# Performance work log

Hardware: AMD Instinct MI355X
Metric: run time of the kernel (lower is better)

The kernel has to match this reference:

```python
import jax, jax.numpy as jnp
from jax import lax
import numpy as np

L, B, D = 2048, 8, 1024
LN_EPS = 1e-5


def setup_inputs() -> dict:
    key = jax.random.key(0)
    k1, k2 = jax.random.split(key)
    x = jax.random.normal(k1, (L, B, D), dtype=jnp.float32)
    c0 = jnp.zeros((B, D), dtype=jnp.float32)
    # nn.Linear(D, 3D, bias=False): weight shape (3D, D), y = x @ W.T
    W = jax.random.normal(k2, (3 * D, D), dtype=jnp.float32) * (1.0 / np.sqrt(D))
    ln_w = jnp.ones((D,), dtype=jnp.float32)
    ln_b = jnp.zeros((D,), dtype=jnp.float32)
    return {"x": x, "c0": c0, "W": W, "ln_w": ln_w, "ln_b": ln_b}


def reference(x, c0, W, ln_w, ln_b):
    # ufr = x @ W.T : (L,B,3D)
    ufr = jnp.einsum('lbd,ed->lbe', x, W)
    u, f, r = jnp.split(ufr, 3, axis=-1)
    f = jax.nn.sigmoid(f)
    r = jax.nn.sigmoid(r)

    # sequential SRU recurrence: c_t = f_t * c_{t-1} + (1 - f_t) * u_t
    def step(c, fu):
        f_t, u_t = fu
        c = f_t * c + (1.0 - f_t) * u_t
        return c, c

    last_c, c_stack = lax.scan(step, c0, (f, u))  # c_stack: (L,B,D)

    hs = r * jnp.tanh(c_stack) + (1.0 - r) * x
    g = jax.nn.gelu(hs, approximate=False)  # torch F.gelu default = exact erf

    mu = jnp.mean(g, axis=-1, keepdims=True)
    var = jnp.mean(jnp.square(g - mu), axis=-1, keepdims=True)
    out = (g - mu) * lax.rsqrt(var + LN_EPS) * ln_w + ln_b
    return (out, last_c)
```

## Files before the change

kernel.cpp:

```cpp
#include <hip/hip_runtime.h>

typedef unsigned short u16;
typedef unsigned int   u32;
typedef __attribute__((ext_vector_type(8))) __bf16 bf16x8;
typedef __attribute__((ext_vector_type(4))) float  f32x4;

#define L_SEQ  2048
#define BATCH  8
#define DIM    1024
#define ROWS   16384
#define N3     3072
#define NCHUNK 64
#define LCHUNK 32
#define NCHAIN 8192

__device__ __forceinline__ float b2f(u16 h) {
  return __builtin_bit_cast(float, (u32)h << 16);
}
__device__ __forceinline__ u32 pk2(float a, float b) {
  u32 r;
  asm("v_cvt_pk_bf16_f32 %0, %1, %2" : "=v"(r) : "v"(a), "v"(b));
  return r;
}
__device__ __forceinline__ u16 f2b(float f) {
  u32 u = __builtin_bit_cast(u32, f);
  return (u16)((u + 0x7fffu + ((u >> 16) & 1u)) >> 16);
}
__device__ __forceinline__ f32x4 mf(bf16x8 a, bf16x8 b, f32x4 c) {
  return __builtin_amdgcn_mfma_f32_16x16x32_bf16(a, b, c, 0, 0, 0);
}

__global__ void k_pack(const float* __restrict__ x, const float* __restrict__ W,
                       u16* __restrict__ apk, u16* __restrict__ wpk) {
  const int NA = 128 * 32 * 8 * 64;
  const int NB = 12 * 32 * 16 * 64;
  int i = blockIdx.x * 256 + threadIdx.x;
  const int stride = gridDim.x * 256;
  for (; i < NA + NB; i += stride) {
    const float* src; u16* dst;
    if (i < NA) {
      int lane = i & 63, fg = (i >> 6) & 7, t = (i >> 9) & 31, mt = i >> 14;
      int row = mt * 128 + fg * 16 + (lane & 15);
      int k   = t * 32 + (lane >> 4) * 8;
      src = x + (size_t)row * DIM + k;
      dst = apk + (size_t)i * 8;
    } else {
      int j = i - NA;
      int lane = j & 63, c = (j >> 6) & 15, t = (j >> 10) & 31, nt = j >> 15;
      int col = nt * 256 + c * 16 + (lane & 15);
      int k   = t * 32 + (lane >> 4) * 8;
      src = W + (size_t)col * DIM + k;
      dst = wpk + (size_t)j * 8;
    }
    float4 v0 = *(const float4*)src;
    float4 v1 = *(const float4*)(src + 4);
    uint4 o;
    o.x = pk2(v0.x, v0.y); o.y = pk2(v0.z, v0.w);
    o.z = pk2(v1.x, v1.y); o.w = pk2(v1.z, v1.w);
    *(uint4*)dst = o;
  }
}

__device__ __forceinline__ void gl_lds16(const u16* g, u16* l) {
  __builtin_amdgcn_global_load_lds((const __attribute__((address_space(1))) void*)g,
                                   (__attribute__((address_space(3))) void*)l,
                                   16, 0, 0);
}

__global__ __launch_bounds__(512, 4) void k_gemm_v6(const u16* __restrict__ apk,
                                                    const u16* __restrict__ wpk,
                                                    u16* __restrict__ C) {
  __shared__ u16 lds[12288];
  const int tid  = threadIdx.x;
  const int lane = tid & 63;
  const int wid  = tid >> 6;
  const int wm = wid >> 2, wn = wid & 3;
  const int lr = lane & 15, lk = lane >> 4;

  const int bid = blockIdx.x;
  const int xcd = bid & 7;
  const int r   = bid >> 3;
  const int byl = r / 12;
  const int bx  = r - byl * 12;
  const int by  = xcd * 16 + byl;

  const u16* srcA = apk + ((((size_t)by * 32) * 8 + wid) * 64 + lane) * 8;
  const u16* srcB = wpk + ((((size_t)bx * 32) * 16 + wn * 4) * 64 + lane) * 8;

  u16* d0 = &lds[wid * 512 + lane * 8];
  u16* d1 = d0 + 4096;
  u16* d2 = d0 + 8192;
  const u16* ldsA = &lds[wm * 2048 + lane * 8];

  f32x4 acc[4][4] = {};
  bf16x8 A0, A1, A2, A3, B0, B1, B2, B3;

  {
    const u16* gb = srcB;
    A0 = *(const bf16x8*)(gb);
    A1 = *(const bf16x8*)(gb + 512);
    A2 = *(const bf16x8*)(gb + 1024);
    A3 = *(const bf16x8*)(gb + 1536);
  }
  __builtin_amdgcn_sched_barrier(0);
  gl_lds16(srcA, d0);
  gl_lds16(srcA + 4096, d1);
  asm volatile("s_waitcnt vmcnt(1)" ::: "memory");
  asm volatile("s_barrier" ::: "memory");

#define GBODY(T, RB, DN, U0,U1,U2,U3, L0,L1,L2,L3, LOADB, STAGEA, LASTP) {   \
    if (STAGEA) gl_lds16(srcA + (size_t)((T) + 2) * 4096, DN);               \
    __builtin_amdgcn_sched_barrier(0);                                       \
    if (LOADB) {                                                             \
      const u16* gb_ = srcB + (size_t)((T) + 1) * 8192;                      \
      L0 = *(const bf16x8*)(gb_);                                            \
      L1 = *(const bf16x8*)(gb_ + 512);                                      \
      L2 = *(const bf16x8*)(gb_ + 1024);                                     \
      L3 = *(const bf16x8*)(gb_ + 1536);                                     \
    }                                                                        \
    __builtin_amdgcn_sched_barrier(0);                                       \
    const u16* rb_ = ldsA + (RB) * 4096;                                     \
    bf16x8 av0 = *(const bf16x8*)(rb_);                                      \
    bf16x8 av1 = *(const bf16x8*)(rb_ + 512);                                \
    bf16x8 av2 = *(const bf16x8*)(rb_ + 1024);                               \
    bf16x8 av3 = *(const bf16x8*)(rb_ + 1536);                               \
    __builtin_amdgcn_s_setprio(1);                                           \
    acc[0][0]=mf(av0,U0,acc[0][0]); acc[0][1]=mf(av0,U1,acc[0][1]);          \
    acc[0][2]=mf(av0,U2,acc[0][2]); acc[0][3]=mf(av0,U3,acc[0][3]);          \
    acc[1][0]=mf(av1,U0,acc[1][0]); acc[1][1]=mf(av1,U1,acc[1][1]);          \
    acc[1][2]=mf(av1,U2,acc[1][2]); acc[1][3]=mf(av1,U3,acc[1][3]);          \
    acc[2][0]=mf(av2,U0,acc[2][0]); acc[2][1]=mf(av2,U1,acc[2][1]);          \
    acc[2][2]=mf(av2,U2,acc[2][2]); acc[2][3]=mf(av2,U3,acc[2][3]);          \
    acc[3][0]=mf(av3,U0,acc[3][0]); acc[3][1]=mf(av3,U1,acc[3][1]);          \
    acc[3][2]=mf(av3,U2,acc[3][2]); acc[3][3]=mf(av3,U3,acc[3][3]);          \
    __builtin_amdgcn_s_setprio(0);                                           \
    if (!(LASTP)) asm volatile("s_barrier" ::: "memory");                    \
  }

  for (int t6 = 0; t6 < 30; t6 += 6) {
    GBODY(t6 + 0, 0, d2, A0,A1,A2,A3, B0,B1,B2,B3, 1, 1, 0)
    GBODY(t6 + 1, 1, d0, B0,B1,B2,B3, A0,A1,A2,A3, 1, 1, 0)
    GBODY(t6 + 2, 2, d1, A0,A1,A2,A3, B0,B1,B2,B3, 1, 1, 0)
    GBODY(t6 + 3, 0, d2, B0,B1,B2,B3, A0,A1,A2,A3, 1, 1, 0)
    GBODY(t6 + 4, 1, d0, A0,A1,A2,A3, B0,B1,B2,B3, 1, 1, 0)
    GBODY(t6 + 5, 2, d1, B0,B1,B2,B3, A0,A1,A2,A3, 1, 1, 0)
  }
  GBODY(30, 0, d2, A0,A1,A2,A3, B0,B1,B2,B3, 1, 0, 0)
  GBODY(31, 1, d0, B0,B1,B2,B3, A0,A1,A2,A3, 0, 0, 1)
#undef GBODY

  const bool act = (bx >= 4);
#pragma unroll
  for (int m = 0; m < 4; ++m) {
    const int row0 = by * 128 + wm * 64 + m * 16 + lk * 4;
#pragma unroll
    for (int n = 0; n < 4; ++n) {
      const int col = bx * 256 + wn * 64 + n * 16 + lr;
#pragma unroll
      for (int j = 0; j < 4; ++j) {
        float v = acc[m][n][j];
        if (act) v = 1.f / (1.f + __expf(-v));
        C[(size_t)(row0 + j) * N3 + col] = f2b(v);
      }
    }
  }
}

__global__ __launch_bounds__(256) void k_gemm_reg(const float* __restrict__ A,
                                                  const float* __restrict__ B,
                                                  u16* __restrict__ C) {
  __shared__ u16 lds[8192];
  const int tid  = threadIdx.x;
  const int lane = tid & 63;
  const int wid  = tid >> 6;
  const int wm = wid >> 1, wn = wid & 1;
  const int lr = lane & 15, lk = lane >> 4;
  const int mBase = blockIdx.y << 7;
  const int nBase = blockIdx.x << 7;

  f32x4 acc[4][4] = {};
  const int aoff = (wm * 64 + lr) * 32 + lk * 8;
  const int boff = 4096 + (wn * 64 + lr) * 32 + lk * 8;

  for (int k0 = 0; k0 < DIM; k0 += 32) {
#pragma unroll
    for (int q = 0; q < 4; ++q) {
      const int i  = q * 256 + tid;
      const int rr = i >> 3;
      const int cc = (i & 7) << 2;
      float4 va = *(const float4*)(A + (size_t)(mBase + rr) * DIM + k0 + cc);
      float4 vb = *(const float4*)(B + (size_t)(nBase + rr) * DIM + k0 + cc);
      uint2 pa; pa.x = pk2(va.x, va.y); pa.y = pk2(va.z, va.w);
      uint2 pb; pb.x = pk2(vb.x, vb.y); pb.y = pk2(vb.z, vb.w);
      *(uint2*)&lds[rr * 32 + cc] = pa;
      *(uint2*)&lds[4096 + rr * 32 + cc] = pb;
    }
    __syncthreads();
    bf16x8 av[4], bv[4];
#pragma unroll
    for (int m = 0; m < 4; ++m) av[m] = *(const bf16x8*)&lds[aoff + m * 512];
#pragma unroll
    for (int n = 0; n < 4; ++n) bv[n] = *(const bf16x8*)&lds[boff + n * 512];
#pragma unroll
    for (int m = 0; m < 4; ++m)
#pragma unroll
      for (int n = 0; n < 4; ++n)
        acc[m][n] = mf(av[m], bv[n], acc[m][n]);
    __syncthreads();
  }

  const bool act = (nBase >= DIM);
#pragma unroll
  for (int m = 0; m < 4; ++m) {
    const int row0 = mBase + wm * 64 + m * 16 + lk * 4;
#pragma unroll
    for (int n = 0; n < 4; ++n) {
      const int col = nBase + wn * 64 + n * 16 + lr;
#pragma unroll
      for (int j = 0; j < 4; ++j) {
        float v = acc[m][n][j];
        if (act) v = 1.f / (1.f + __expf(-v));
        C[(size_t)(row0 + j) * N3 + col] = f2b(v);
      }
    }
  }
}

__global__ void k_scanA(const u16* __restrict__ ufr, float* __restrict__ P,
                        float* __restrict__ V) {
  int g = blockIdx.x * 256 + threadIdx.x;
  int j = g >> 13;
  int chain = g & (NCHAIN - 1);
  int b = chain >> 10;
  int d = chain & (DIM - 1);
  const u16* p = ufr + (size_t)((j * LCHUNK) * BATCH + b) * N3 + d;
  float prod = 1.f, v = 0.f;
  for (int t = 0; t < LCHUNK; ++t) {
    float u = b2f(p[0]);
    float f = b2f(p[DIM]);
    v = f * v + (1.f - f) * u;
    prod *= f;
    p += BATCH * N3;
  }
  P[g] = prod; V[g] = v;
}

__global__ void k_scanB(const float* __restrict__ c0, const float* __restrict__ P,
                        const float* __restrict__ V, float* __restrict__ S,
                        float* __restrict__ lastc) {
  int chain = blockIdx.x * 256 + threadIdx.x;
  float c = c0[chain];
  for (int j = 0; j < NCHUNK; ++j) {
    S[j * NCHAIN + chain] = c;
    c = P[j * NCHAIN + chain] * c + V[j * NCHAIN + chain];
  }
  lastc[chain] = c;
}

__global__ __launch_bounds__(1024) void k_scanln(const u16* __restrict__ ufr,
                                                 const float* __restrict__ S,
                                                 const float* __restrict__ x,
                                                 const float* __restrict__ lnw,
                                                 const float* __restrict__ lnb,
                                                 float* __restrict__ out) {
  const int j = blockIdx.x >> 3;
  const int b = blockIdx.x & 7;
  const int d = threadIdx.x;
  const int lane = d & 63, wid = d >> 6;

  float c = S[j * NCHAIN + b * DIM + d];
  const float wgt = lnw[d];
  const float bia = lnb[d];

  const u16*   pu = ufr + (size_t)((j * LCHUNK) * BATCH + b) * N3 + d;
  const float* px = x   + (size_t)((j * LCHUNK) * BATCH + b) * DIM + d;
  float*       po = out + (size_t)((j * LCHUNK) * BATCH + b) * DIM + d;

  __shared__ float red1[16], red2[16];

  u16 cu = pu[0], cf = pu[DIM], cr = pu[2 * DIM];
  float cx = *px;

  for (int t = 0; t < LCHUNK; ++t) {
    const int adv = (t < LCHUNK - 1) ? 1 : 0;
    u16 nu = pu[(size_t)adv * BATCH * N3];
    u16 nf = pu[(size_t)adv * BATCH * N3 + DIM];
    u16 nr = pu[(size_t)adv * BATCH * N3 + 2 * DIM];
    float nx = px[(size_t)adv * BATCH * DIM];

    float u = b2f(cu), f = b2f(cf), rr = b2f(cr), xx = cx;
    c = f * c + (1.f - f) * u;
    float hs = rr * tanhf(c) + (1.f - rr) * xx;
    float g  = 0.5f * hs * (1.f + erff(hs * 0.70710678118654752f));

    float s1 = g, s2 = g * g;
#pragma unroll
    for (int off = 32; off > 0; off >>= 1) {
      s1 += __shfl_down(s1, off, 64);
      s2 += __shfl_down(s2, off, 64);
    }
    if (lane == 0) { red1[wid] = s1; red2[wid] = s2; }
    __syncthreads();
    float S1 = 0.f, S2 = 0.f;
#pragma unroll
    for (int w = 0; w < 16; ++w) { S1 += red1[w]; S2 += red2[w]; }
    float mu  = S1 * (1.f / DIM);
    float var = S2 * (1.f / DIM) - mu * mu;
    float inv = rsqrtf(var + 1e-5f);
    *po = (g - mu) * inv * wgt + bia;
    __syncthreads();

    cu = nu; cf = nf; cr = nr; cx = nx;
    pu += BATCH * N3;
    px += BATCH * DIM;
    po += BATCH * DIM;
  }
}

extern "C" void kernel_launch(void* const* d_in, const int* in_sizes, int n_in,
                              void* d_out, int out_size, void* d_ws, size_t ws_size,
                              hipStream_t stream) {
  (void)in_sizes; (void)n_in; (void)out_size;
  const float* x   = (const float*)d_in[0];
  const float* c0  = (const float*)d_in[1];
  const float* W   = (const float*)d_in[2];
  const float* lnw = (const float*)d_in[3];
  const float* lnb = (const float*)d_in[4];
  float* out   = (float*)d_out;
  float* lastc = out + (size_t)ROWS * DIM;

  char* ws = (char*)d_ws;

  u16* ufr; float *P, *V, *S;
  const size_t FULL_NEED = 140509184;
  if (ws_size >= FULL_NEED) {
    u16* apk = (u16*)ws;
    u16* wpk = (u16*)(ws + 33554432);
    ufr = (u16*)(ws + 39845888);
    P   = (float*)ws;
    V   = (float*)(ws + 2097152);
    S   = (float*)(ws + 4194304);
    k_pack<<<2048, 256, 0, stream>>>(x, W, apk, wpk);
    k_gemm_v6<<<1536, 512, 0, stream>>>(apk, wpk, ufr);
  } else {
    ufr = (u16*)ws;
    P   = (float*)(ws + 100663296);
    V   = (float*)(ws + 102760448);
    S   = (float*)(ws + 104857600);
    dim3 g1(N3 / 128, ROWS / 128);
    k_gemm_reg<<<g1, 256, 0, stream>>>(x, W, ufr);
  }

  k_scanA<<<(NCHUNK * NCHAIN) / 256, 256, 0, stream>>>(ufr, P, V);
  k_scanB<<<NCHAIN / 256, 256, 0, stream>>>(c0, P, V, S, lastc);
  k_scanln<<<NCHUNK * BATCH, 1024, 0, stream>>>(ufr, S, x, lnw, lnb, out);
}
```

Measured before the change: 234.4 us.

## Vectorize scan kernels to four channels per thread and halve chunk length

```diff
diff --git a/kernel.cpp b/kernel.cpp
--- a/kernel.cpp
+++ b/kernel.cpp
@@ -10,9 +10,11 @@
 #define DIM    1024
 #define ROWS   16384
 #define N3     3072
-#define NCHUNK 64
-#define LCHUNK 32
+#define NCHUNK 128
+#define LCHUNK 16
 #define NCHAIN 8192
+
+struct __align__(8) us4 { u16 x, y, z, w; };
 
 __device__ __forceinline__ float b2f(u16 h) {
   return __builtin_bit_cast(float, (u32)h << 16);
@@ -228,21 +230,27 @@
 
 __global__ void k_scanA(const u16* __restrict__ ufr, float* __restrict__ P,
                         float* __restrict__ V) {
-  int g = blockIdx.x * 256 + threadIdx.x;
-  int j = g >> 13;
-  int chain = g & (NCHAIN - 1);
-  int b = chain >> 10;
-  int d = chain & (DIM - 1);
-  const u16* p = ufr + (size_t)((j * LCHUNK) * BATCH + b) * N3 + d;
-  float prod = 1.f, v = 0.f;
+  int idx = blockIdx.x * 256 + threadIdx.x;
+  int j  = idx >> 11;
+  int cg = idx & 2047;
+  int b  = cg >> 8;
+  int d0 = (cg & 255) << 2;
+  const u16* p = ufr + (size_t)((j * LCHUNK) * BATCH + b) * N3 + d0;
+  float prod0 = 1.f, prod1 = 1.f, prod2 = 1.f, prod3 = 1.f;
+  float v0 = 0.f, v1 = 0.f, v2 = 0.f, v3 = 0.f;
   for (int t = 0; t < LCHUNK; ++t) {
-    float u = b2f(p[0]);
-    float f = b2f(p[DIM]);
-    v = f * v + (1.f - f) * u;
-    prod *= f;
+    us4 uu = *(const us4*)(p);
+    us4 ff = *(const us4*)(p + DIM);
+    float f0 = b2f(ff.x), f1 = b2f(ff.y), f2 = b2f(ff.z), f3 = b2f(ff.w);
+    v0 = f0 * v0 + (1.f - f0) * b2f(uu.x); prod0 *= f0;
+    v1 = f1 * v1 + (1.f - f1) * b2f(uu.y); prod1 *= f1;
+    v2 = f2 * v2 + (1.f - f2) * b2f(uu.z); prod2 *= f2;
+    v3 = f3 * v3 + (1.f - f3) * b2f(uu.w); prod3 *= f3;
     p += BATCH * N3;
   }
-  P[g] = prod; V[g] = v;
+  const int base = j * NCHAIN + b * DIM + d0;
+  *(float4*)&P[base] = make_float4(prod0, prod1, prod2, prod3);
+  *(float4*)&V[base] = make_float4(v0, v1, v2, v3);
 }
 
 __global__ void k_scanB(const float* __restrict__ c0, const float* __restrict__ P,
@@ -257,58 +265,89 @@
   lastc[chain] = c;
 }
 
-__global__ __launch_bounds__(1024) void k_scanln(const u16* __restrict__ ufr,
-                                                 const float* __restrict__ S,
-                                                 const float* __restrict__ x,
-                                                 const float* __restrict__ lnw,
-                                                 const float* __restrict__ lnb,
-                                                 float* __restrict__ out) {
+__global__ __launch_bounds__(256) void k_scanln(const u16* __restrict__ ufr,
+                                                const float* __restrict__ S,
+                                                const float* __restrict__ x,
+                                                const float* __restrict__ lnw,
+                                                const float* __restrict__ lnb,
+                                                float* __restrict__ out) {
   const int j = blockIdx.x >> 3;
   const int b = blockIdx.x & 7;
-  const int d = threadIdx.x;
-  const int lane = d & 63, wid = d >> 6;
-
-  float c = S[j * NCHAIN + b * DIM + d];
-  const float wgt = lnw[d];
-  const float bia = lnb[d];
-
-  const u16*   pu = ufr + (size_t)((j * LCHUNK) * BATCH + b) * N3 + d;
-  const float* px = x   + (size_t)((j * LCHUNK) * BATCH + b) * DIM + d;
-  float*       po = out + (size_t)((j * LCHUNK) * BATCH + b) * DIM + d;
-
-  __shared__ float red1[16], red2[16];
-
-  u16 cu = pu[0], cf = pu[DIM], cr = pu[2 * DIM];
-  float cx = *px;
+  const int tid = threadIdx.x;
+  const int d0 = tid << 2;
+  const int lane = tid & 63, wid = tid >> 6;
+
+  float4 c4  = *(const float4*)&S[j * NCHAIN + b * DIM + d0];
+  float c0v = c4.x, c1v = c4.y, c2v = c4.z, c3v = c4.w;
+  const float4 wv = *(const float4*)(lnw + d0);
+  const float4 bv = *(const float4*)(lnb + d0);
+
+  const u16*   pu = ufr + (size_t)((j * LCHUNK) * BATCH + b) * N3 + d0;
+  const float* px = x   + (size_t)((j * LCHUNK) * BATCH + b) * DIM + d0;
+  float*       po = out + (size_t)((j * LCHUNK) * BATCH + b) * DIM + d0;
+
+  __shared__ float red1[2][4], red2[2][4];
+
+  us4 cu = *(const us4*)(pu);
+  us4 cf = *(const us4*)(pu + DIM);
+  us4 cr = *(const us4*)(pu + 2 * DIM);
+  float4 cx = *(const float4*)px;
 
   for (int t = 0; t < LCHUNK; ++t) {
-    const int adv = (t < LCHUNK - 1) ? 1 : 0;
-    u16 nu = pu[(size_t)adv * BATCH * N3];
-    u16 nf = pu[(size_t)adv * BATCH * N3 + DIM];
-    u16 nr = pu[(size_t)adv * BATCH * N3 + 2 * DIM];
-    float nx = px[(size_t)adv * BATCH * DIM];
-
-    float u = b2f(cu), f = b2f(cf), rr = b2f(cr), xx = cx;
-    c = f * c + (1.f - f) * u;
-    float hs = rr * tanhf(c) + (1.f - rr) * xx;
-    float g  = 0.5f * hs * (1.f + erff(hs * 0.70710678118654752f));
-
-    float s1 = g, s2 = g * g;
+    const size_t advU = (t < LCHUNK - 1) ? (size_t)BATCH * N3 : 0;
+    const size_t advX = (t < LCHUNK - 1) ? (size_t)BATCH * DIM : 0;
+    us4 nu = *(const us4*)(pu + advU);
+    us4 nf = *(const us4*)(pu + advU + DIM);
+    us4 nr = *(const us4*)(pu + advU + 2 * DIM);
+    float4 nx = *(const float4*)(px + advX);
+
+    float g0, g1, g2, g3;
+    {
+      float f = b2f(cf.x); c0v = f * c0v + (1.f - f) * b2f(cu.x);
+      float rr = b2f(cr.x);
+      float hs = rr * tanhf(c0v) + (1.f - rr) * cx.x;
+      g0 = 0.5f * hs * (1.f + erff(hs * 0.70710678118654752f));
+    }
+    {
+      float f = b2f(cf.y); c1v = f * c1v + (1.f - f) * b2f(cu.y);
+      float rr = b2f(cr.y);
+      float hs = rr * tanhf(c1v) + (1.f - rr) * cx.y;
+      g1 = 0.5f * hs * (1.f + erff(hs * 0.70710678118654752f));
+    }
+    {
+      float f = b2f(cf.z); c2v = f * c2v + (1.f - f) * b2f(cu.z);
+      float rr = b2f(cr.z);
+      float hs = rr * tanhf(c2v) + (1.f - rr) * cx.z;
+      g2 = 0.5f * hs * (1.f + erff(hs * 0.70710678118654752f));
+    }
+    {
+      float f = b2f(cf.w); c3v = f * c3v + (1.f - f) * b2f(cu.w);
+      float rr = b2f(cr.w);
+      float hs = rr * tanhf(c3v) + (1.f - rr) * cx.w;
+      g3 = 0.5f * hs * (1.f + erff(hs * 0.70710678118654752f));
+    }
+
+    float s1 = g0 + g1 + g2 + g3;
+    float s2 = g0 * g0 + g1 * g1 + g2 * g2 + g3 * g3;
 #pragma unroll
     for (int off = 32; off > 0; off >>= 1) {
       s1 += __shfl_down(s1, off, 64);
       s2 += __shfl_down(s2, off, 64);
     }
-    if (lane == 0) { red1[wid] = s1; red2[wid] = s2; }
+    const int pb = t & 1;
+    if (lane == 0) { red1[pb][wid] = s1; red2[pb][wid] = s2; }
     __syncthreads();
-    float S1 = 0.f, S2 = 0.f;
-#pragma unroll
-    for (int w = 0; w < 16; ++w) { S1 += red1[w]; S2 += red2[w]; }
+    float S1 = red1[pb][0] + red1[pb][1] + red1[pb][2] + red1[pb][3];
+    float S2 = red2[pb][0] + red2[pb][1] + red2[pb][2] + red2[pb][3];
     float mu  = S1 * (1.f / DIM);
     float var = S2 * (1.f / DIM) - mu * mu;
     float inv = rsqrtf(var + 1e-5f);
-    *po = (g - mu) * inv * wgt + bia;
-    __syncthreads();
+    float4 o;
+    o.x = (g0 - mu) * inv * wv.x + bv.x;
+    o.y = (g1 - mu) * inv * wv.y + bv.y;
+    o.z = (g2 - mu) * inv * wv.z + bv.z;
+    o.w = (g3 - mu) * inv * wv.w + bv.w;
+    *(float4*)po = o;
 
     cu = nu; cf = nf; cr = nr; cx = nx;
     pu += BATCH * N3;
@@ -338,20 +377,20 @@
     u16* wpk = (u16*)(ws + 33554432);
     ufr = (u16*)(ws + 39845888);
     P   = (float*)ws;
-    V   = (float*)(ws + 2097152);
-    S   = (float*)(ws + 4194304);
+    V   = (float*)(ws + 4194304);
+    S   = (float*)(ws + 8388608);
     k_pack<<<2048, 256, 0, stream>>>(x, W, apk, wpk);
     k_gemm_v6<<<1536, 512, 0, stream>>>(apk, wpk, ufr);
   } else {
     ufr = (u16*)ws;
     P   = (float*)(ws + 100663296);
-    V   = (float*)(ws + 102760448);
-    S   = (float*)(ws + 104857600);
+    V   = (float*)(ws + 104857600);
+    S   = (float*)(ws + 109051904);
     dim3 g1(N3 / 128, ROWS / 128);
     k_gemm_reg<<<g1, 256, 0, stream>>>(x, W, ufr);
   }
 
-  k_scanA<<<(NCHUNK * NCHAIN) / 256, 256, 0, stream>>>(ufr, P, V);
+  k_scanA<<<1024, 256, 0, stream>>>(ufr, P, V);
   k_scanB<<<NCHAIN / 256, 256, 0, stream>>>(c0, P, V, S, lastc);
-  k_scanln<<<NCHUNK * BATCH, 1024, 0, stream>>>(ufr, S, x, lnw, lnb, out);
-}
+  k_scanln<<<NCHUNK * BATCH, 256, 0, stream>>>(ufr, S, x, lnw, lnb, out);
+}
```

Result: faster. 190.5 us, median of 2 (-18.7%).
